# Kernel tuning notes

Hardware: AMD Instinct MI355X
Metric: run time of the kernel (lower is better)

## Reference

```python
import jax, jax.numpy as jnp
import numpy as np

IN_CHANNELS = (256, 512)
SPATIAL = ((64, 64), (32, 32))
BATCH = 4
CORR = 5          # corr_size (patch_size of spatial_correlation_sample)
SEQ = 4           # gating_seq_len
PAD = (CORR - 1) // 2


def conv3x3(x, w, b):
    # NCHW conv, 3x3, stride 1, pad 1 (== padding='SAME')
    y = jax.lax.conv_general_dilated(x, w, (1, 1), 'SAME',
                                     dimension_numbers=('NCHW', 'OIHW', 'NCHW'))
    return y + b[None, :, None, None]


def align(feat2, feat1):
    # spatial_correlation_sample(feat2, feat1, kernel_size=1, patch_size=CORR,
    # padding=0, dilation_patch=1): corr[b,i,j,y,x] = sum_c feat2[b,c,y,x] *
    # feat1[b,c,y+i-PAD,x+j-PAD] (zero outside). Then softmax over the 25
    # offsets with scale 20/corr.max(), then the unrolled shifted-slice warp.
    b, c, h, w = feat1.shape
    pad1 = jnp.pad(feat1, ((0, 0), (0, 0), (PAD, PAD), (PAD, PAD)))
    corr = jnp.stack(
        [jnp.einsum('bchw,bchw->bhw', feat2, pad1[:, :, i:i + h, j:j + w])
         for i in range(CORR) for j in range(CORR)], axis=1)  # [b, 25, h, w]
    # note: any constant channel-normalization of the correlation cancels in
    # the 20/corr.max() scaling, so plain channel-sum is faithful.
    att = jax.nn.softmax(corr * (20.0 / corr.max()), axis=1)
    new = jnp.zeros_like(feat1)
    k = 0
    for i in range(CORR):
        for j in range(CORR):
            new = new + att[:, k:k + 1] * pad1[:, :, i:i + h, j:j + w]
            k += 1
    return new


def level_forward(frames, Wg, bg, Wd, bd, Wc, bc):
    # frames: list of SEQ feature maps [b,C,h,w]; key frame is frames[SEQ-1]
    key_f = frames[SEQ - 1]
    gated = []
    for s in range(SEQ - 1):
        new = align(key_f, frames[s])
        feat = jnp.concatenate([key_f, new], axis=1)           # [b, 2C, h, w]
        g = jax.nn.sigmoid(conv3x3(feat, Wg[s], bg[s]))        # [b, 2, h, w]
        fg = jnp.concatenate([key_f * g[:, 0:1], new * g[:, 1:2]], axis=1)
        gated.append(jax.nn.relu(conv3x3(fg, Wd[s], bd[s])))   # [b, C, h, w]
    total = jnp.concatenate(gated, axis=1)                     # [b, 3C, h, w]
    return jax.nn.relu(conv3x3(total, Wc, bc))


def setup_inputs() -> dict:
    key = jax.random.key(0)
    ks = iter(jax.random.split(key, 64))
    inp = {}
    for s in range(SEQ):
        for l, (c, (h, w)) in enumerate(zip(IN_CHANNELS, SPATIAL)):
            inp[f"x{s}{l}"] = jax.random.normal(next(ks), (BATCH, c, h, w), jnp.float32) * 0.1
    for l, c in enumerate(IN_CHANNELS):
        fan = float(1.0 / np.sqrt(2 * c * 9))
        inp[f"Wg{l}"] = jax.random.uniform(next(ks), (SEQ - 1, 2, 2 * c, 3, 3), jnp.float32, -fan, fan)
        inp[f"bg{l}"] = jnp.zeros((SEQ - 1, 2), jnp.float32)
        inp[f"Wd{l}"] = jax.random.uniform(next(ks), (SEQ - 1, c, 2 * c, 3, 3), jnp.float32, -fan, fan)
        inp[f"bd{l}"] = jnp.zeros((SEQ - 1, c), jnp.float32)
        fan3 = float(1.0 / np.sqrt(3 * c * 9))
        inp[f"Wc{l}"] = jax.random.uniform(next(ks), (c, 3 * c, 3, 3), jnp.float32, -fan3, fan3)
        inp[f"bc{l}"] = jnp.zeros((c,), jnp.float32)
    return inp


def reference(x00, x01, x10, x11, x20, x21, x30, x31,
              Wg0, bg0, Wd0, bd0, Wc0, bc0,
              Wg1, bg1, Wd1, bd1, Wc1, bc1):
    out0 = level_forward([x00, x10, x20, x30], Wg0, bg0, Wd0, bd0, Wc0, bc0)
    out1 = level_forward([x01, x11, x21, x31], Wg1, bg1, Wd1, bd1, Wc1, bc1)
    return (out0, out1)
```

## Files before the change

kernel.cpp:

```cpp
#include <hip/hip_runtime.h>
#include <hip/hip_bf16.h>
#include <math.h>

#define PAD 2

typedef __attribute__((ext_vector_type(8))) short s8v;
typedef __attribute__((ext_vector_type(4))) float f4v;

__device__ __forceinline__ f4v mfma16(s8v a, s8v b, f4v c){
    return __builtin_amdgcn_mfma_f32_16x16x32_bf16(a, b, c, 0, 0, 0);
}

__device__ __forceinline__ unsigned short f2bf(float f){
    unsigned u = __float_as_uint(f);
    unsigned r = u + 0x7FFFu + ((u >> 16) & 1u);
    return (unsigned short)(r >> 16);
}

__device__ __forceinline__ unsigned f2o(float f){
    unsigned b = __float_as_uint(f);
    return (b & 0x80000000u) ? ~b : (b | 0x80000000u);
}
__device__ __forceinline__ float o2f(unsigned u){
    return __uint_as_float((u & 0x80000000u) ? (u & 0x7fffffffu) : ~u);
}

__device__ __forceinline__ float bperm(int adr, float v){
    return __uint_as_float((unsigned)__builtin_amdgcn_ds_bpermute(adr, (int)__float_as_uint(v)));
}

__global__ __launch_bounds__(256)
void corr_v2(const float* __restrict__ key, const float* __restrict__ frame,
             float* __restrict__ corr,
             int C, int CW, int H, int W, int logHW, int logW){
    const int tid = threadIdx.x, lane = tid & 63, wv = tid >> 6;
    const int HW = 1 << logHW;
    const int p0 = blockIdx.x * 64;
    const int b  = p0 >> logHW;
    const int remL = (p0 & (HW - 1)) + lane;
    const int y = remL >> logW, x = remL & (W - 1);

    float m[25];
    #pragma unroll
    for (int t = 0; t < 25; t++){
        const int dy = t / 5 - 2, dx = t % 5 - 2;
        m[t] = (((unsigned)(y + dy) < (unsigned)H) &&
                ((unsigned)(x + dx) < (unsigned)W)) ? 1.f : 0.f;
    }
    int adr[4];
    const int dxs[4] = {-2, -1, 1, 2};
    #pragma unroll
    for (int i = 0; i < 4; i++) adr[i] = ((lane + dxs[i]) & 63) << 2;

    int roff[5];
    #pragma unroll
    for (int r = 0; r < 5; r++){
        const int dy = r - 2;
        roff[r] = ((unsigned)(y + dy) < (unsigned)H) ? dy * W : 0;
    }

    const int c0 = (blockIdx.y * 4 + wv) * CW;
    const float* kp = key   + (((size_t)b * C + c0) << logHW) + remL;
    const float* fp = frame + (((size_t)b * C + c0) << logHW) + remL;

    float acc[25];
    #pragma unroll
    for (int t = 0; t < 25; t++) acc[t] = 0.f;

    for (int ci = 0; ci < CW; ci++){
        const float k = kp[0];
        float f[5];
        #pragma unroll
        for (int r = 0; r < 5; r++) f[r] = fp[roff[r]];
        #pragma unroll
        for (int r = 0; r < 5; r++){
            float v[5];
            v[0] = bperm(adr[0], f[r]);
            v[1] = bperm(adr[1], f[r]);
            v[2] = f[r];
            v[3] = bperm(adr[2], f[r]);
            v[4] = bperm(adr[3], f[r]);
            #pragma unroll
            for (int j = 0; j < 5; j++)
                acc[r * 5 + j] += k * (v[j] * m[r * 5 + j]);
        }
        kp += HW; fp += HW;
    }

    __shared__ float sacc[4][25][64];
    #pragma unroll
    for (int t = 0; t < 25; t++) sacc[wv][t][lane] = acc[t];
    __syncthreads();
    #pragma unroll
    for (int tg = 0; tg < 7; tg++){
        const int t = wv + tg * 4;
        if (t < 25){
            const float s = sacc[0][t][lane] + sacc[1][t][lane] +
                            sacc[2][t][lane] + sacc[3][t][lane];
            atomicAdd(corr + (((size_t)b * 25 + t) << logHW) + remL, s);
        }
    }
}

__global__ void max_kernel(const float* __restrict__ corr, unsigned* __restrict__ gmax){
    float v = corr[(size_t)blockIdx.x * 256 + threadIdx.x];
    #pragma unroll
    for (int o = 32; o > 0; o >>= 1) v = fmaxf(v, __shfl_down(v, o));
    if ((threadIdx.x & 63) == 0) atomicMax(gmax, f2o(v));
}

__global__ void att_kernel(float* __restrict__ corr, const unsigned* __restrict__ gmax,
                           int logHW){
    const int p = blockIdx.x * 256 + threadIdx.x;
    const int b = p >> logHW;
    const int rem = p & ((1 << logHW) - 1);
    float* cp = corr + (((size_t)b * 25) << logHW) + rem;
    const float scale = 20.f / o2f(*gmax);

    float z[25]; float m = -INFINITY;
    #pragma unroll
    for (int k = 0; k < 25; k++){
        z[k] = cp[k << logHW] * scale;
        m = fmaxf(m, z[k]);
    }
    float s = 0.f;
    #pragma unroll
    for (int k = 0; k < 25; k++){ z[k] = expf(z[k] - m); s += z[k]; }
    const float inv = 1.f / s;
    #pragma unroll
    for (int k = 0; k < 25; k++) cp[k << logHW] = z[k] * inv;
}

__global__ __launch_bounds__(256)
void warp_v2(const float* __restrict__ frame, const float* __restrict__ att,
             float* __restrict__ newf,
             int C, int CW, int H, int W, int logHW, int logW){
    const int tid = threadIdx.x, lane = tid & 63, wv = tid >> 6;
    const int HW = 1 << logHW;
    const int p0 = blockIdx.x * 64;
    const int b  = p0 >> logHW;
    const int remL = (p0 & (HW - 1)) + lane;
    const int y = remL >> logW, x = remL & (W - 1);

    int adr[4];
    const int dxs[4] = {-2, -1, 1, 2};
    #pragma unroll
    for (int i = 0; i < 4; i++) adr[i] = ((lane + dxs[i]) & 63) << 2;

    int roff[5];
    #pragma unroll
    for (int r = 0; r < 5; r++){
        const int dy = r - 2;
        roff[r] = ((unsigned)(y + dy) < (unsigned)H) ? dy * W : 0;
    }

    const float* ap = att + (((size_t)b * 25) << logHW) + remL;
    float a[25];
    #pragma unroll
    for (int t = 0; t < 25; t++){
        const int dy = t / 5 - 2, dx = t % 5 - 2;
        const float mk = (((unsigned)(y + dy) < (unsigned)H) &&
                          ((unsigned)(x + dx) < (unsigned)W)) ? 1.f : 0.f;
        a[t] = ap[(size_t)t << logHW] * mk;
    }

    const int c0 = (blockIdx.y * 4 + wv) * CW;
    const float* fp = frame + (((size_t)b * C + c0) << logHW) + remL;
    float*       op = newf  + (((size_t)b * C + c0) << logHW) + remL;

    for (int ci = 0; ci < CW; ci++){
        float f[5];
        #pragma unroll
        for (int r = 0; r < 5; r++) f[r] = fp[roff[r]];
        float acc = 0.f;
        #pragma unroll
        for (int r = 0; r < 5; r++){
            float v[5];
            v[0] = bperm(adr[0], f[r]);
            v[1] = bperm(adr[1], f[r]);
            v[2] = f[r];
            v[3] = bperm(adr[2], f[r]);
            v[4] = bperm(adr[3], f[r]);
            #pragma unroll
            for (int j = 0; j < 5; j++)
                acc += a[r * 5 + j] * v[j];
        }
        op[0] = acc;
        fp += HW; op += HW;
    }
}

__global__ __launch_bounds__(256)
void gate_v2(const float* __restrict__ key, const float* __restrict__ newf,
             const float* __restrict__ Wg, float* __restrict__ gz,
             int C, int CW, int H, int W, int logHW, int logW){
    const int tid = threadIdx.x, lane = tid & 63, wv = tid >> 6;
    const int HW = 1 << logHW;
    const int p0 = blockIdx.x * 64;
    const int b  = p0 >> logHW;
    const int remL = (p0 & (HW - 1)) + lane;
    const int y = remL >> logW, x = remL & (W - 1);

    float m[9];
    #pragma unroll
    for (int t = 0; t < 9; t++){
        const int dy = t / 3 - 1, dx = t % 3 - 1;
        m[t] = (((unsigned)(y + dy) < (unsigned)H) &&
                ((unsigned)(x + dx) < (unsigned)W)) ? 1.f : 0.f;
    }
    const int adrL = ((lane - 1) & 63) << 2;
    const int adrR = ((lane + 1) & 63) << 2;

    int roff[3];
    #pragma unroll
    for (int r = 0; r < 3; r++){
        const int dy = r - 1;
        roff[r] = ((unsigned)(y + dy) < (unsigned)H) ? dy * W : 0;
    }

    const int c0 = (blockIdx.y * 4 + wv) * CW;
    const float* base = (c0 < C)
        ? key  + (((size_t)b * C + c0)       << logHW)
        : newf + (((size_t)b * C + (c0 - C)) << logHW);
    const float* ip = base + remL;

    float z0 = 0.f, z1 = 0.f;
    for (int ci = 0; ci < CW; ci++){
        const int u = c0 + ci;
        const float* w0 = Wg + (size_t)u * 9;
        const float* w1 = Wg + ((size_t)2 * C + u) * 9;
        float f[3];
        #pragma unroll
        for (int r = 0; r < 3; r++) f[r] = ip[roff[r]];
        #pragma unroll
        for (int r = 0; r < 3; r++){
            float v[3];
            v[0] = bperm(adrL, f[r]);
            v[1] = f[r];
            v[2] = bperm(adrR, f[r]);
            #pragma unroll
            for (int j = 0; j < 3; j++){
                const float val = v[j] * m[r * 3 + j];
                z0 += val * w0[r * 3 + j];
                z1 += val * w1[r * 3 + j];
            }
        }
        ip += HW;
    }

    __shared__ float sz[2][4][64];
    sz[0][wv][lane] = z0; sz[1][wv][lane] = z1;
    __syncthreads();
    if (wv < 2){
        const float s = sz[wv][0][lane] + sz[wv][1][lane] +
                        sz[wv][2][lane] + sz[wv][3][lane];
        atomicAdd(gz + ((size_t)b * 2 + wv) * HW + remL, s);
    }
}

__global__ void prep_gin(const float* __restrict__ key, const float* __restrict__ newf,
                         const float* __restrict__ g, const float* __restrict__ bg,
                         unsigned short* __restrict__ gin,
                         int C, int HW){
    __shared__ unsigned short tile[64][65];
    int tid = threadIdx.x;
    int pt0 = blockIdx.x * 64;
    int u0  = blockIdx.y * 64;
    int b   = pt0 / HW;
    int rem0 = pt0 - b * HW;
    const float* gb = g + (size_t)(b * 2) * HW;

    #pragma unroll
    for (int it = 0; it < 16; it++){
        int idx = it * 256 + tid;
        int ur = idx >> 6, pc = idx & 63;
        int u = u0 + ur; int rem = rem0 + pc;
        const float* src; int sel;
        if (u < C){ src = key  + ((size_t)b * C + u) * HW;       sel = 0; }
        else      { src = newf + ((size_t)b * C + (u - C)) * HW; sel = 1; }
        float zz = gb[(size_t)sel * HW + rem] + bg[sel];
        float gv = 1.f / (1.f + expf(-zz));
        float v = src[rem] * gv;
        tile[ur][pc] = f2bf(v);
    }
    __syncthreads();
    unsigned short* go = gin + (size_t)pt0 * (2 * C) + u0;
    #pragma unroll
    for (int it = 0; it < 16; it++){
        int idx = it * 256 + tid;
        int pr = idx >> 6, uc = idx & 63;
        go[(size_t)pr * (2 * C) + uc] = tile[uc][pr];
    }
}

__global__ void prep_w(const float* __restrict__ W, unsigned short* __restrict__ Wt,
                       int Cin){
    int ci = blockIdx.y * 256 + threadIdx.x;
    int bx = blockIdx.x;
    int co = bx / 9, t = bx - co * 9;
    Wt[(size_t)bx * Cin + ci] = f2bf(W[((size_t)co * Cin + ci) * 9 + t]);
}

template<int BN, int EPI>
__global__ __launch_bounds__(256, 2)
void conv_mfma(const unsigned short* __restrict__ gin,
               const unsigned short* __restrict__ Wt,
               const float* __restrict__ bias,
               unsigned short* __restrict__ obf, int ostride,
               float* __restrict__ of32,
               const void* __restrict__ zp,
               int Cin, int Cout, int H, int W, int logHW, int logW)
{
    constexpr int BM = 64;
    constexpr int BNh = BN / 2;
    constexpr int NJ = BN / 32;
    __shared__ __align__(16) unsigned short sA[4][BM * 32];
    __shared__ __align__(16) unsigned short sB[4][BN * 32];

    const int tid = threadIdx.x;
    const int lane = tid & 63;
    const int wv = tid >> 6;
    const int wm = wv >> 1, wn = wv & 1;
    const int ln = lane & 15, q = lane >> 4;

    const int p0 = blockIdx.x * BM;
    const int b  = p0 >> logHW;
    const int rem0 = p0 - (b << logHW);

    const int rowA0 = tid >> 2;
    const int gc8 = ((tid & 3) ^ ((tid >> 3) & 3)) * 8;
    const int remA0 = rem0 + rowA0;
    const int yA0 = remA0 >> logW, xA0 = remA0 & (W - 1);
    const size_t pbase = ((size_t)b << logHW);

    const int nt0 = blockIdx.y * BN;
    const size_t Ktot = (size_t)9 * Cin;
    const unsigned short* wB0 = Wt + (size_t)(nt0 + rowA0) * Ktot + gc8;

    f4v acc[2][NJ];
    #pragma unroll
    for (int i = 0; i < 2; i++)
        #pragma unroll
        for (int j = 0; j < NJ; j++){ f4v z = {0.f, 0.f, 0.f, 0.f}; acc[i][j] = z; }

    const int cblocks = Cin >> 5;
    const int total = 9 * cblocks;
    const int npairs = total >> 1;

    int scb = 0;
    int st  = 0;
    bool sv = (yA0 > 0) && (xA0 > 0);
    const unsigned short* sa  = gin + (pbase + remA0 + (-W - 1)) * Cin + gc8;
    const unsigned short* swb = wB0;

    struct Regs { f4v a, b0, b1; };
    Regs R0, R1, R2, R3;

    auto issue1 = [&](Regs& r){
        r.a  = *(const f4v*)(sv ? (const void*)(sa + scb * 32) : zp);
        r.b0 = *(const f4v*)swb;
        if constexpr (BN == 128) r.b1 = *(const f4v*)(swb + (size_t)64 * Ktot);
        swb += 32;
        if (++scb == cblocks){
            scb = 0; ++st;
            const int dy = st / 3 - 1, dx = st - (st / 3) * 3 - 1;
            sv = ((unsigned)(yA0 + dy) < (unsigned)H) && ((unsigned)(xA0 + dx) < (unsigned)W);
            sa = gin + (pbase + remA0 + dy * W + dx) * Cin + gc8;
        }
    };
    auto commit1 = [&](const Regs& r, int buf){
        *(f4v*)((char*)sA[buf] + (size_t)tid * 16) = r.a;
        char* dB = (char*)sB[buf];
        *(f4v*)(dB + (size_t)tid * 16) = r.b0;
        if constexpr (BN == 128) *(f4v*)(dB + 4096 + (size_t)tid * 16) = r.b1;
    };

    const int rchunk = (q ^ ((ln >> 1) & 3)) * 8;
    auto compute1 = [&](int buf){
        const unsigned short* A = sA[buf];
        const unsigned short* B = sB[buf];
        s8v af[2];
        #pragma unroll
        for (int i = 0; i < 2; i++)
            af[i] = *(const s8v*)(A + (wm * 32 + i * 16 + ln) * 32 + rchunk);
        __builtin_amdgcn_s_setprio(1);
        #pragma unroll
        for (int j = 0; j < NJ; j++){
            s8v bfr = *(const s8v*)(B + (wn * BNh + j * 16 + ln) * 32 + rchunk);
            #pragma unroll
            for (int i = 0; i < 2; i++)
                acc[i][j] = mfma16(af[i], bfr, acc[i][j]);
        }
        __builtin_amdgcn_s_setprio(0);
    };

    #define WAIT_CUR()  do{ if constexpr (BN == 128) asm volatile("s_waitcnt vmcnt(6)" ::: "memory"); \
                            else                     asm volatile("s_waitcnt vmcnt(4)" ::: "memory"); }while(0)
    #define WAIT_ALL()  asm volatile("s_waitcnt vmcnt(0)" ::: "memory")

    issue1(R0); issue1(R1); issue1(R2); issue1(R3);

    for (int t = 0; t < npairs; t += 2){
        if (t + 1 < npairs) WAIT_CUR(); else WAIT_ALL();
        __builtin_amdgcn_sched_barrier(0);
        commit1(R0, 0); commit1(R1, 1);
        if (t + 2 < npairs){ issue1(R0); issue1(R1); }
        asm volatile("s_waitcnt lgkmcnt(0)" ::: "memory");
        __builtin_amdgcn_sched_barrier(0);
        __builtin_amdgcn_s_barrier();
        compute1(0); compute1(1);

        if (t + 2 < npairs) WAIT_CUR(); else WAIT_ALL();
        __builtin_amdgcn_sched_barrier(0);
        commit1(R2, 2); commit1(R3, 3);
        if (t + 3 < npairs){ issue1(R2); issue1(R3); }
        asm volatile("s_waitcnt lgkmcnt(0)" ::: "memory");
        __builtin_amdgcn_sched_barrier(0);
        __builtin_amdgcn_s_barrier();
        compute1(2); compute1(3);
    }
    #undef WAIT_CUR
    #undef WAIT_ALL

    #pragma unroll
    for (int i = 0; i < 2; i++){
        const int m0 = wm * 32 + i * 16 + q * 4;
        const int p = p0 + m0;
        #pragma unroll
        for (int j = 0; j < NJ; j++){
            const int n = nt0 + wn * BNh + j * 16 + ln;
            const float bv = bias[n];
            if (EPI == 0){
                #pragma unroll
                for (int r = 0; r < 4; r++){
                    float v = fmaxf(acc[i][j][r] + bv, 0.f);
                    obf[(size_t)(p + r) * ostride + n] = f2bf(v);
                }
            } else {
                f4v o;
                #pragma unroll
                for (int r = 0; r < 4; r++) o[r] = fmaxf(acc[i][j][r] + bv, 0.f);
                const int rem = rem0 + m0;
                *(f4v*)(of32 + (((size_t)b * Cout + n) << logHW) + rem) = o;
            }
        }
    }
}

extern "C" void kernel_launch(void* const* d_in, const int* in_sizes, int n_in,
                              void* d_out, int out_size, void* d_ws, size_t ws_size,
                              hipStream_t stream){
    (void)in_sizes; (void)n_in; (void)out_size; (void)ws_size;

    const float* X[4][2];
    for (int s = 0; s < 4; s++)
        for (int l = 0; l < 2; l++)
            X[s][l] = (const float*)d_in[s * 2 + l];
    const float* Wg[2] = { (const float*)d_in[8],  (const float*)d_in[14] };
    const float* bg[2] = { (const float*)d_in[9],  (const float*)d_in[15] };
    const float* Wd[2] = { (const float*)d_in[10], (const float*)d_in[16] };
    const float* bd[2] = { (const float*)d_in[11], (const float*)d_in[17] };
    const float* Wc[2] = { (const float*)d_in[12], (const float*)d_in[18] };
    const float* bc[2] = { (const float*)d_in[13], (const float*)d_in[19] };
    float* out = (float*)d_out;

    char* ws = (char*)d_ws;
    unsigned* gmax = (unsigned*)ws;
    const void* zp = (const void*)(ws + 1024);
    float* corrbuf = (float*)(ws + 4096);
    float* newbuf  = (float*)(ws + 4096 + 1638400);
    unsigned short* wtbuf = (unsigned short*)newbuf;
    float* gbuf    = (float*)(ws + 4096 + 1638400 + 16777216);
    unsigned short* ginbuf = (unsigned short*)(ws + 4096 + 1638400 + 16777216 + 131072);
    unsigned short* totbuf = (unsigned short*)(ws + 4096 + 1638400 + 16777216 + 131072 + 16777216);

    hipMemsetAsync(ws, 0, 4096, stream);

    const int Cs[2] = {256, 512};
    const int Hs[2] = {64, 32};
    const int logWs[2] = {6, 5};
    const int logHWs[2] = {12, 10};
    const size_t outOff[2] = {0, (size_t)4 * 256 * 4096};

    for (int l = 0; l < 2; l++){
        const int C = Cs[l], H = Hs[l], W = Hs[l], HW = H * W;
        const int logW = logWs[l], logHW = logHWs[l];
        const float* key = X[3][l];
        const int pblk = 4 * HW / 256;
        const int Mt = 4 * HW / 64;

        const int gx  = 4 * HW / 64;
        const int S   = (l == 0) ? 2 : 8;
        const int CWc = C / (4 * S);
        const int CWg = (2 * C) / (4 * S);

        for (int s = 0; s < 3; s++){
            const float* fr = X[s][l];
            unsigned* slot = gmax + (l * 3 + s);
            hipMemsetAsync(corrbuf, 0, (size_t)4 * 25 * HW * 4, stream);
            hipMemsetAsync(gbuf,    0, (size_t)4 * 2 * HW * 4, stream);
            corr_v2<<<dim3(gx, S), 256, 0, stream>>>(
                key, fr, corrbuf, C, CWc, H, W, logHW, logW);
            max_kernel<<<25 * 4 * HW / 256, 256, 0, stream>>>(corrbuf, slot);
            att_kernel<<<pblk, 256, 0, stream>>>(corrbuf, slot, logHW);
            warp_v2<<<dim3(gx, S), 256, 0, stream>>>(
                fr, corrbuf, newbuf, C, CWc, H, W, logHW, logW);
            gate_v2<<<dim3(gx, S), 256, 0, stream>>>(
                key, newbuf, Wg[l] + (size_t)s * 2 * (2 * C) * 9,
                gbuf, C, CWg, H, W, logHW, logW);
            prep_gin<<<dim3(4 * HW / 64, 2 * C / 64), 256, 0, stream>>>(
                key, newbuf, gbuf, bg[l] + (size_t)s * 2, ginbuf, C, HW);
            prep_w<<<dim3(C * 9, 2 * C / 256), 256, 0, stream>>>(
                Wd[l] + (size_t)s * C * 2 * C * 9, wtbuf, 2 * C);
            if (l == 0)
                conv_mfma<128, 0><<<dim3(Mt, C / 128), 256, 0, stream>>>(
                    ginbuf, wtbuf, bd[l] + s * C, totbuf + s * C, 3 * C,
                    nullptr, zp, 2 * C, C, H, W, logHW, logW);
            else
                conv_mfma<64, 0><<<dim3(Mt, C / 64), 256, 0, stream>>>(
                    ginbuf, wtbuf, bd[l] + s * C, totbuf + s * C, 3 * C,
                    nullptr, zp, 2 * C, C, H, W, logHW, logW);
        }
        prep_w<<<dim3(C * 9, 3 * C / 256), 256, 0, stream>>>(Wc[l], wtbuf, 3 * C);
        if (l == 0)
            conv_mfma<128, 1><<<dim3(Mt, 2), 256, 0, stream>>>(
                totbuf, wtbuf, bc[l], nullptr, 0,
                out + outOff[l], zp, 3 * C, C, H, W, logHW, logW);
        else
            conv_mfma<64, 1><<<dim3(Mt, 8), 256, 0, stream>>>(
                totbuf, wtbuf, bc[l], nullptr, 0,
                out + outOff[l], zp, 3 * C, C, H, W, logHW, logW);
    }
}
```

Baseline: 1.796 ms.

## Shrink conv MFMA tiles to 32 rows with 2-wave blocks and XCD-aware grid mapping

The implicit-GEMM conv kernel now uses 128-thread blocks (two waves split only along N) with a 32-pixel M tile instead of 64, doubling the number of workgroups. It also flattens the grid into 1D and remaps block IDs so that workgroups landing on the same XCD share weight or activation tiles for better L2 locality. The aim is more parallelism and better cache reuse per XCD, at the cost of less A-tile reuse per block and more B loads per thread, with vmcnt waits retuned to match.

```diff
diff --git a/kernel.cpp b/kernel.cpp
--- a/kernel.cpp
+++ b/kernel.cpp
@@ -302,28 +302,35 @@
 }
 
 template<int BN, int EPI>
-__global__ __launch_bounds__(256, 2)
+__global__ __launch_bounds__(128, 2)
 void conv_mfma(const unsigned short* __restrict__ gin,
                const unsigned short* __restrict__ Wt,
                const float* __restrict__ bias,
                unsigned short* __restrict__ obf, int ostride,
                float* __restrict__ of32,
                const void* __restrict__ zp,
-               int Cin, int Cout, int H, int W, int logHW, int logW)
+               int Cin, int Cout, int H, int W, int logHW, int logW,
+               int Mt, int Ny)
 {
-    constexpr int BM = 64;
+    constexpr int BM = 32;
     constexpr int BNh = BN / 2;
     constexpr int NJ = BN / 32;
+    constexpr int NR = BN / 32;
     __shared__ __align__(16) unsigned short sA[4][BM * 32];
     __shared__ __align__(16) unsigned short sB[4][BN * 32];
 
     const int tid = threadIdx.x;
     const int lane = tid & 63;
-    const int wv = tid >> 6;
-    const int wm = wv >> 1, wn = wv & 1;
+    const int wn = tid >> 6;
     const int ln = lane & 15, q = lane >> 4;
 
-    const int p0 = blockIdx.x * BM;
+    const int wgid = blockIdx.x;
+    int xt, yt;
+    if (Ny == 8){ yt = wgid & 7; xt = wgid >> 3; }
+    else        { const int xcd = wgid & 7; yt = xcd >> 2;
+                  xt = (xcd & 3) * (Mt >> 2) + (wgid >> 3); }
+
+    const int p0 = xt * BM;
     const int b  = p0 >> logHW;
     const int rem0 = p0 - (b << logHW);
 
@@ -333,7 +340,7 @@
     const int yA0 = remA0 >> logW, xA0 = remA0 & (W - 1);
     const size_t pbase = ((size_t)b << logHW);
 
-    const int nt0 = blockIdx.y * BN;
+    const int nt0 = yt * BN;
     const size_t Ktot = (size_t)9 * Cin;
     const unsigned short* wB0 = Wt + (size_t)(nt0 + rowA0) * Ktot + gc8;
 
@@ -353,13 +360,14 @@
     const unsigned short* sa  = gin + (pbase + remA0 + (-W - 1)) * Cin + gc8;
     const unsigned short* swb = wB0;
 
-    struct Regs { f4v a, b0, b1; };
+    struct Regs { f4v a; f4v bb[NR]; };
     Regs R0, R1, R2, R3;
 
     auto issue1 = [&](Regs& r){
-        r.a  = *(const f4v*)(sv ? (const void*)(sa + scb * 32) : zp);
-        r.b0 = *(const f4v*)swb;
-        if constexpr (BN == 128) r.b1 = *(const f4v*)(swb + (size_t)64 * Ktot);
+        r.a = *(const f4v*)(sv ? (const void*)(sa + scb * 32) : zp);
+        #pragma unroll
+        for (int rd = 0; rd < NR; rd++)
+            r.bb[rd] = *(const f4v*)(swb + (size_t)rd * 32 * Ktot);
         swb += 32;
         if (++scb == cblocks){
             scb = 0; ++st;
@@ -371,8 +379,9 @@
     auto commit1 = [&](const Regs& r, int buf){
         *(f4v*)((char*)sA[buf] + (size_t)tid * 16) = r.a;
         char* dB = (char*)sB[buf];
-        *(f4v*)(dB + (size_t)tid * 16) = r.b0;
-        if constexpr (BN == 128) *(f4v*)(dB + 4096 + (size_t)tid * 16) = r.b1;
+        #pragma unroll
+        for (int rd = 0; rd < NR; rd++)
+            *(f4v*)(dB + rd * 2048 + (size_t)tid * 16) = r.bb[rd];
     };
 
     const int rchunk = (q ^ ((ln >> 1) & 3)) * 8;
@@ -382,7 +391,7 @@
         s8v af[2];
         #pragma unroll
         for (int i = 0; i < 2; i++)
-            af[i] = *(const s8v*)(A + (wm * 32 + i * 16 + ln) * 32 + rchunk);
+            af[i] = *(const s8v*)(A + (i * 16 + ln) * 32 + rchunk);
         __builtin_amdgcn_s_setprio(1);
         #pragma unroll
         for (int j = 0; j < NJ; j++){
@@ -394,8 +403,8 @@
         __builtin_amdgcn_s_setprio(0);
     };
 
-    #define WAIT_CUR()  do{ if constexpr (BN == 128) asm volatile("s_waitcnt vmcnt(6)" ::: "memory"); \
-                            else                     asm volatile("s_waitcnt vmcnt(4)" ::: "memory"); }while(0)
+    #define WAIT_CUR()  do{ if constexpr (BN == 128) asm volatile("s_waitcnt vmcnt(10)" ::: "memory"); \
+                            else                     asm volatile("s_waitcnt vmcnt(6)" ::: "memory"); }while(0)
     #define WAIT_ALL()  asm volatile("s_waitcnt vmcnt(0)" ::: "memory")
 
     issue1(R0); issue1(R1); issue1(R2); issue1(R3);
@@ -424,7 +433,7 @@
 
     #pragma unroll
     for (int i = 0; i < 2; i++){
-        const int m0 = wm * 32 + i * 16 + q * 4;
+        const int m0 = i * 16 + q * 4;
         const int p = p0 + m0;
         #pragma unroll
         for (int j = 0; j < NJ; j++){
@@ -487,12 +496,14 @@
         const int logW = logWs[l], logHW = logHWs[l];
         const float* key = X[3][l];
         const int pblk = 4 * HW / 256;
-        const int Mt = 4 * HW / 64;
+        const int Mt = 4 * HW / 32;
 
         const int gx  = 4 * HW / 64;
         const int S   = (l == 0) ? 2 : 8;
         const int CWc = C / (4 * S);
         const int CWg = (2 * C) / (4 * S);
+
+        const int Ny  = (l == 0) ? 2 : 8;
 
         for (int s = 0; s < 3; s++){
             const float* fr = X[s][l];
@@ -513,22 +524,22 @@
             prep_w<<<dim3(C * 9, 2 * C / 256), 256, 0, stream>>>(
                 Wd[l] + (size_t)s * C * 2 * C * 9, wtbuf, 2 * C);
             if (l == 0)
-                conv_mfma<128, 0><<<dim3(Mt, C / 128), 256, 0, stream>>>(
+                conv_mfma<128, 0><<<dim3(Mt * Ny), 128, 0, stream>>>(
                     ginbuf, wtbuf, bd[l] + s * C, totbuf + s * C, 3 * C,
-                    nullptr, zp, 2 * C, C, H, W, logHW, logW);
+                    nullptr, zp, 2 * C, C, H, W, logHW, logW, Mt, Ny);
             else
-                conv_mfma<64, 0><<<dim3(Mt, C / 64), 256, 0, stream>>>(
+                conv_mfma<64, 0><<<dim3(Mt * Ny), 128, 0, stream>>>(
                     ginbuf, wtbuf, bd[l] + s * C, totbuf + s * C, 3 * C,
-                    nullptr, zp, 2 * C, C, H, W, logHW, logW);
+                    nullptr, zp, 2 * C, C, H, W, logHW, logW, Mt, Ny);
         }
         prep_w<<<dim3(C * 9, 3 * C / 256), 256, 0, stream>>>(Wc[l], wtbuf, 3 * C);
         if (l == 0)
-            conv_mfma<128, 1><<<dim3(Mt, 2), 256, 0, stream>>>(
+            conv_mfma<128, 1><<<dim3(Mt * Ny), 128, 0, stream>>>(
                 totbuf, wtbuf, bc[l], nullptr, 0,
-                out + outOff[l], zp, 3 * C, C, H, W, logHW, logW);
+                out + outOff[l], zp, 3 * C, C, H, W, logHW, logW, Mt, Ny);
         else
-            conv_mfma<64, 1><<<dim3(Mt, 8), 256, 0, stream>>>(
+            conv_mfma<64, 1><<<dim3(Mt * Ny), 128, 0, stream>>>(
                 totbuf, wtbuf, bc[l], nullptr, 0,
-                out + outOff[l], zp, 3 * C, C, H, W, logHW, logW);
-    }
-}
+                out + outOff[l], zp, 3 * C, C, H, W, logHW, logW, Mt, Ny);
+    }
+}
```

Result: slower. 1.977 ms (+10.1%).
